# Performance work log

Measured on AMD Instinct MI355X. Metric: run time of the kernel, lower is better.

The kernel has to match this reference:

```python
import jax, jax.numpy as jnp
import numpy as np
import math

MSG_DIM = 128
ATT_DIM = 128
N = 20000
KN = 32  # neighbors per node


def setup_inputs() -> dict:
    key = jax.random.key(0)
    ks = jax.random.split(key, 8)
    s = 1.0 / math.sqrt(MSG_DIM)
    return {
        "query_msg": jax.random.normal(ks[0], (N, MSG_DIM), dtype=jnp.float32),
        "neighbor_msgs": jax.random.normal(ks[1], (N, KN, MSG_DIM), dtype=jnp.float32),
        # nn.Linear params: weight [out, in], bias [out]
        "Wq": jax.random.uniform(ks[2], (ATT_DIM, MSG_DIM), jnp.float32, -s, s),
        "bq": jax.random.uniform(ks[3], (ATT_DIM,), jnp.float32, -s, s),
        "Wk": jax.random.uniform(ks[4], (ATT_DIM, MSG_DIM), jnp.float32, -s, s),
        "bk": jax.random.uniform(ks[5], (ATT_DIM,), jnp.float32, -s, s),
        "Wv": jax.random.uniform(ks[6], (MSG_DIM, MSG_DIM), jnp.float32, -s, s),
        "bv": jax.random.uniform(ks[7], (MSG_DIM,), jnp.float32, -s, s),
    }


def reference(query_msg, neighbor_msgs, Wq, bq, Wk, bk, Wv, bv):
    scale = math.sqrt(ATT_DIM)
    Q = query_msg @ Wq.T + bq                       # [N, att_dim]
    K = jnp.einsum('nkd,ad->nka', neighbor_msgs, Wk) + bk  # [N, K, att_dim]
    V = jnp.einsum('nkd,md->nkm', neighbor_msgs, Wv) + bv  # [N, K, msg_dim]
    scores = jnp.einsum('na,nka->nk', Q, K) / scale  # [N, K]
    att = jax.nn.softmax(scores, axis=1)             # softmax over neighbors
    return jnp.einsum('nk,nkm->nm', att, V)          # [N, msg_dim]
```

## Files before the change

### kernel.cpp

```cpp
#include <hip/hip_runtime.h>
#include <math.h>

#define MSG 128
#define KN 32

__global__ void gac_prep(const float* __restrict__ Wq, const float* __restrict__ bq,
                         const float* __restrict__ Wk,
                         float* __restrict__ Mp, float* __restrict__ cp) {
    const float inv_scale = 0.088388347648318440f;
    const int d = blockIdx.x;
    const int e = threadIdx.x;
    float acc = 0.f;
#pragma unroll 8
    for (int a = 0; a < 128; ++a)
        acc = fmaf(Wk[a * 128 + d], Wq[a * 128 + e], acc);
    Mp[d * 128 + e] = acc * inv_scale;

    if (threadIdx.x < 64) {
        const int l = threadIdx.x;
        float p = Wk[l * 128 + d] * bq[l] + Wk[(l + 64) * 128 + d] * bq[l + 64];
#pragma unroll
        for (int off = 32; off; off >>= 1) p += __shfl_down(p, off, 64);
        if (l == 0) cp[d] = p * inv_scale;
    }
}

__global__ __launch_bounds__(256, 4)
void gac_fused(const float* __restrict__ query,
               const float* __restrict__ nbr,
               const float* __restrict__ Mp,
               const float* __restrict__ cp,
               const float* __restrict__ Wv,
               const float* __restrict__ bv,
               float* __restrict__ out, int N) {
    __shared__ __align__(16) float bufA[16 * 128];
    __shared__ __align__(16) float q2[16 * 128];
    __shared__ __align__(16) float part[2 * 16 * 128];

    const int t = threadIdx.x;
    const int r = t & 127;
    const int h = t >> 7;
    const int w = t >> 6;
    const int l = t & 63;

    const int n0 = blockIdx.x * 16;
    const size_t maxf4 = (size_t)N * 32 - 1;

    {
        const float4* src = (const float4*)query;
        size_t i0 = (size_t)n0 * 32 + t;
        size_t i1 = i0 + 256;
        ((float4*)bufA)[t]       = src[i0 > maxf4 ? maxf4 : i0];
        ((float4*)bufA)[t + 256] = src[i1 > maxf4 ? maxf4 : i1];
    }
    __syncthreads();

    {
        float4 wA[16];
        const float4* wp = (const float4*)(Mp + r * 128 + h * 64);
#pragma unroll
        for (int i = 0; i < 16; ++i) wA[i] = wp[i];
        const float br = (h == 0) ? cp[r] : 0.f;
        float acc[16];
#pragma unroll
        for (int j = 0; j < 16; ++j) acc[j] = br;
#pragma unroll
        for (int i = 0; i < 16; ++i) {
            const float4 w4 = wA[i];
#pragma unroll
            for (int j = 0; j < 16; ++j) {
                const float4 q4 = ((const float4*)(bufA + j * 128 + h * 64))[i];
                acc[j] = fmaf(w4.x, q4.x, acc[j]);
                acc[j] = fmaf(w4.y, q4.y, acc[j]);
                acc[j] = fmaf(w4.z, q4.z, acc[j]);
                acc[j] = fmaf(w4.w, q4.w, acc[j]);
            }
        }
#pragma unroll
        for (int j = 0; j < 16; ++j) part[h * 2048 + j * 128 + r] = acc[j];
    }
    __syncthreads();
#pragma unroll
    for (int i = 0; i < 8; ++i) {
        const int e = t + 256 * i;
        q2[e] = part[e] + part[2048 + e];
    }
    __syncthreads();

#pragma unroll 1
    for (int jj = 0; jj < 4; ++jj) {
        const int ln = 4 * w + jj;
        int n = n0 + ln;
        if (n >= N) n = N - 1;
        const float* x = nbr + (size_t)n * KN * MSG;
        float2 xv[KN];
#pragma unroll
        for (int k = 0; k < KN; ++k)
            xv[k] = ((const float2*)(x + k * MSG))[l];
        const float2 qq = ((const float2*)(q2 + ln * 128))[l];

        float s = 0.f;
        const int myk = l & 31;
#pragma unroll
        for (int k = 0; k < KN; ++k) {
            float p = fmaf(xv[k].y, qq.y, xv[k].x * qq.x);
#pragma unroll
            for (int off = 32; off; off >>= 1) p += __shfl_xor(p, off, 64);
            if (myk == k) s = p;
        }
        float m = s;
#pragma unroll
        for (int off = 16; off; off >>= 1) m = fmaxf(m, __shfl_xor(m, off, 64));
        const float e = __expf(s - m);
        float sum = e;
#pragma unroll
        for (int off = 16; off; off >>= 1) sum += __shfl_xor(sum, off, 64);
        const float a = e / sum;
        float2 c = make_float2(0.f, 0.f);
#pragma unroll
        for (int k = 0; k < KN; ++k) {
            const float ak = __shfl(a, k, 64);
            c.x = fmaf(ak, xv[k].x, c.x);
            c.y = fmaf(ak, xv[k].y, c.y);
        }
        ((float2*)(bufA + ln * 128))[l] = c;
    }
    __syncthreads();

    {
        float4 wV[16];
        const float4* wp = (const float4*)(Wv + r * 128 + h * 64);
#pragma unroll
        for (int i = 0; i < 16; ++i) wV[i] = wp[i];
        const float br = (h == 0) ? bv[r] : 0.f;
        float acc[16];
#pragma unroll
        for (int j = 0; j < 16; ++j) acc[j] = br;
#pragma unroll
        for (int i = 0; i < 16; ++i) {
            const float4 w4 = wV[i];
#pragma unroll
            for (int j = 0; j < 16; ++j) {
                const float4 c4 = ((const float4*)(bufA + j * 128 + h * 64))[i];
                acc[j] = fmaf(w4.x, c4.x, acc[j]);
                acc[j] = fmaf(w4.y, c4.y, acc[j]);
                acc[j] = fmaf(w4.z, c4.z, acc[j]);
                acc[j] = fmaf(w4.w, c4.w, acc[j]);
            }
        }
#pragma unroll
        for (int j = 0; j < 16; ++j) part[h * 2048 + j * 128 + r] = acc[j];
    }
    __syncthreads();
#pragma unroll
    for (int i = 0; i < 8; ++i) {
        const int e = t + 256 * i;
        const size_t idx = (size_t)n0 * 128 + e;
        if (idx < (size_t)N * 128) out[idx] = part[e] + part[2048 + e];
    }
}

extern "C" void kernel_launch(void* const* d_in, const int* in_sizes, int n_in,
                              void* d_out, int out_size, void* d_ws, size_t ws_size,
                              hipStream_t stream) {
    const float* query = (const float*)d_in[0];
    const float* nbr   = (const float*)d_in[1];
    const float* Wq    = (const float*)d_in[2];
    const float* bq    = (const float*)d_in[3];
    const float* Wk    = (const float*)d_in[4];
    const float* Wv    = (const float*)d_in[6];
    const float* bv    = (const float*)d_in[7];
    float* out = (float*)d_out;

    const int N = in_sizes[0] / MSG;

    float* Mp = (float*)d_ws;
    float* cp = Mp + 128 * 128;

    gac_prep<<<128, 128, 0, stream>>>(Wq, bq, Wk, Mp, cp);

    const int grid = (N + 15) / 16;
    gac_fused<<<grid, 256, 0, stream>>>(query, nbr, Mp, cp, Wv, bv, out, N);
}
```

Baseline: 503.1 us.

## Load neighbor rows as float4 with nontemporal hints and half-wave neighbor split

Neighbor messages are now read as 16-byte nontemporal vector loads, with each half-wave covering 16 neighbors using 4 channels per lane, instead of float2 loads over all 32 neighbors. This shortens each score reduction to a 5-step shuffle and halves the per-lane weighted-sum loop, at the cost of one extra cross-half shuffle to combine the output. The partial-sum combine and output store are vectorized to float4, and the output store is nontemporal. The aim is fewer memory instructions and shuffles on this bandwidth-bound stream, while keeping the same per-lane register footprint.

```diff
diff --git a/kernel.cpp b/kernel.cpp
--- a/kernel.cpp
+++ b/kernel.cpp
@@ -3,6 +3,8 @@
 
 #define MSG 128
 #define KN 32
+
+typedef float vf4 __attribute__((ext_vector_type(4)));
 
 __global__ void gac_prep(const float* __restrict__ Wq, const float* __restrict__ bq,
                          const float* __restrict__ Wk,
@@ -47,17 +49,17 @@
     const size_t maxf4 = (size_t)N * 32 - 1;
 
     {
-        const float4* src = (const float4*)query;
+        const vf4* src = (const vf4*)query;
         size_t i0 = (size_t)n0 * 32 + t;
         size_t i1 = i0 + 256;
-        ((float4*)bufA)[t]       = src[i0 > maxf4 ? maxf4 : i0];
-        ((float4*)bufA)[t + 256] = src[i1 > maxf4 ? maxf4 : i1];
+        ((vf4*)bufA)[t]       = __builtin_nontemporal_load(src + (i0 > maxf4 ? maxf4 : i0));
+        ((vf4*)bufA)[t + 256] = __builtin_nontemporal_load(src + (i1 > maxf4 ? maxf4 : i1));
     }
     __syncthreads();
 
     {
-        float4 wA[16];
-        const float4* wp = (const float4*)(Mp + r * 128 + h * 64);
+        vf4 wA[16];
+        const vf4* wp = (const vf4*)(Mp + r * 128 + h * 64);
 #pragma unroll
         for (int i = 0; i < 16; ++i) wA[i] = wp[i];
         const float br = (h == 0) ? cp[r] : 0.f;
@@ -66,10 +68,10 @@
         for (int j = 0; j < 16; ++j) acc[j] = br;
 #pragma unroll
         for (int i = 0; i < 16; ++i) {
-            const float4 w4 = wA[i];
+            const vf4 w4 = wA[i];
 #pragma unroll
             for (int j = 0; j < 16; ++j) {
-                const float4 q4 = ((const float4*)(bufA + j * 128 + h * 64))[i];
+                const vf4 q4 = ((const vf4*)(bufA + j * 128 + h * 64))[i];
                 acc[j] = fmaf(w4.x, q4.x, acc[j]);
                 acc[j] = fmaf(w4.y, q4.y, acc[j]);
                 acc[j] = fmaf(w4.z, q4.z, acc[j]);
@@ -81,9 +83,11 @@
     }
     __syncthreads();
 #pragma unroll
-    for (int i = 0; i < 8; ++i) {
-        const int e = t + 256 * i;
-        q2[e] = part[e] + part[2048 + e];
+    for (int i = 0; i < 2; ++i) {
+        const int e4 = t + 256 * i;
+        const vf4 pa = ((const vf4*)part)[e4];
+        const vf4 pb = ((const vf4*)(part + 2048))[e4];
+        ((vf4*)q2)[e4] = pa + pb;
     }
     __syncthreads();
 
@@ -92,44 +96,67 @@
         const int ln = 4 * w + jj;
         int n = n0 + ln;
         if (n >= N) n = N - 1;
-        const float* x = nbr + (size_t)n * KN * MSG;
-        float2 xv[KN];
-#pragma unroll
-        for (int k = 0; k < KN; ++k)
-            xv[k] = ((const float2*)(x + k * MSG))[l];
-        const float2 qq = ((const float2*)(q2 + ln * 128))[l];
+        const vf4* x4 = (const vf4*)(nbr + (size_t)n * KN * MSG);
+        vf4 xv[16];
+#pragma unroll
+        for (int i = 0; i < 16; ++i)
+            xv[i] = __builtin_nontemporal_load(x4 + i * 64 + l);
+        const vf4 qq = ((const vf4*)(q2 + ln * 128))[l & 31];
 
         float s = 0.f;
-        const int myk = l & 31;
-#pragma unroll
-        for (int k = 0; k < KN; ++k) {
-            float p = fmaf(xv[k].y, qq.y, xv[k].x * qq.x);
-#pragma unroll
-            for (int off = 32; off; off >>= 1) p += __shfl_xor(p, off, 64);
-            if (myk == k) s = p;
+        const int li = l & 15;
+#pragma unroll
+        for (int i = 0; i < 16; ++i) {
+            float p = xv[i].x * qq.x;
+            p = fmaf(xv[i].y, qq.y, p);
+            p = fmaf(xv[i].z, qq.z, p);
+            p = fmaf(xv[i].w, qq.w, p);
+            p += __shfl_xor(p, 16, 64);
+            p += __shfl_xor(p, 8, 64);
+            p += __shfl_xor(p, 4, 64);
+            p += __shfl_xor(p, 2, 64);
+            p += __shfl_xor(p, 1, 64);
+            if (li == i) s = p;
         }
         float m = s;
-#pragma unroll
-        for (int off = 16; off; off >>= 1) m = fmaxf(m, __shfl_xor(m, off, 64));
+        m = fmaxf(m, __shfl_xor(m, 8, 64));
+        m = fmaxf(m, __shfl_xor(m, 4, 64));
+        m = fmaxf(m, __shfl_xor(m, 2, 64));
+        m = fmaxf(m, __shfl_xor(m, 1, 64));
+        m = fmaxf(m, __shfl_xor(m, 32, 64));
         const float e = __expf(s - m);
         float sum = e;
-#pragma unroll
-        for (int off = 16; off; off >>= 1) sum += __shfl_xor(sum, off, 64);
+        sum += __shfl_xor(sum, 8, 64);
+        sum += __shfl_xor(sum, 4, 64);
+        sum += __shfl_xor(sum, 2, 64);
+        sum += __shfl_xor(sum, 1, 64);
+        sum += __shfl_xor(sum, 32, 64);
         const float a = e / sum;
-        float2 c = make_float2(0.f, 0.f);
-#pragma unroll
-        for (int k = 0; k < KN; ++k) {
-            const float ak = __shfl(a, k, 64);
-            c.x = fmaf(ak, xv[k].x, c.x);
-            c.y = fmaf(ak, xv[k].y, c.y);
-        }
-        ((float2*)(bufA + ln * 128))[l] = c;
+
+        float cx = 0.f, cy = 0.f, cz = 0.f, cw = 0.f;
+        const int half = l & 32;
+#pragma unroll
+        for (int i = 0; i < 16; ++i) {
+            const float ak = __shfl(a, i + half, 64);
+            cx = fmaf(ak, xv[i].x, cx);
+            cy = fmaf(ak, xv[i].y, cy);
+            cz = fmaf(ak, xv[i].z, cz);
+            cw = fmaf(ak, xv[i].w, cw);
+        }
+        cx += __shfl_xor(cx, 32, 64);
+        cy += __shfl_xor(cy, 32, 64);
+        cz += __shfl_xor(cz, 32, 64);
+        cw += __shfl_xor(cw, 32, 64);
+        if (l < 32) {
+            vf4 c; c.x = cx; c.y = cy; c.z = cz; c.w = cw;
+            ((vf4*)(bufA + ln * 128))[l] = c;
+        }
     }
     __syncthreads();
 
     {
-        float4 wV[16];
-        const float4* wp = (const float4*)(Wv + r * 128 + h * 64);
+        vf4 wV[16];
+        const vf4* wp = (const vf4*)(Wv + r * 128 + h * 64);
 #pragma unroll
         for (int i = 0; i < 16; ++i) wV[i] = wp[i];
         const float br = (h == 0) ? bv[r] : 0.f;
@@ -138,10 +165,10 @@
         for (int j = 0; j < 16; ++j) acc[j] = br;
 #pragma unroll
         for (int i = 0; i < 16; ++i) {
-            const float4 w4 = wV[i];
+            const vf4 w4 = wV[i];
 #pragma unroll
             for (int j = 0; j < 16; ++j) {
-                const float4 c4 = ((const float4*)(bufA + j * 128 + h * 64))[i];
+                const vf4 c4 = ((const vf4*)(bufA + j * 128 + h * 64))[i];
                 acc[j] = fmaf(w4.x, c4.x, acc[j]);
                 acc[j] = fmaf(w4.y, c4.y, acc[j]);
                 acc[j] = fmaf(w4.z, c4.z, acc[j]);
@@ -153,10 +180,14 @@
     }
     __syncthreads();
 #pragma unroll
-    for (int i = 0; i < 8; ++i) {
-        const int e = t + 256 * i;
-        const size_t idx = (size_t)n0 * 128 + e;
-        if (idx < (size_t)N * 128) out[idx] = part[e] + part[2048 + e];
+    for (int i = 0; i < 2; ++i) {
+        const int e4 = t + 256 * i;
+        const vf4 pa = ((const vf4*)part)[e4];
+        const vf4 pb = ((const vf4*)(part + 2048))[e4];
+        const vf4 v = pa + pb;
+        const size_t idx4 = (size_t)n0 * 32 + e4;
+        if (idx4 < (size_t)N * 32)
+            __builtin_nontemporal_store(v, (vf4*)out + idx4);
     }
 }
 
```

Measured after the change: 456.7 us. 1.1x faster.
